# Kernel optimization log

Measured on AMD Instinct MI355X. Metric: run time of the kernel, lower is better.

The kernel has to match this reference:

```python
import jax, jax.numpy as jnp
import numpy as np

NUM_GRAPHS = 64


def gcn_conv(x, W, b, row, col, ew, n_nodes):
    # PyG GCNConv with edge weights: add self-loops (weight 1), symmetric norm.
    deg = jax.ops.segment_sum(ew, col, num_segments=n_nodes) + 1.0  # self-loop weight
    dis = jnp.where(deg > 0, jax.lax.rsqrt(deg), 0.0)
    norm = dis[row] * ew * dis[col]  # [E]
    xw = x @ W  # [N, H]
    # edge messages aggregated at target (col) + self-loop contribution dis_i^2 * xw_i
    agg = jnp.zeros_like(xw).at[col].add(norm[:, None] * xw[row])
    agg = agg + (dis * dis)[:, None] * xw
    return agg + b


def reference(x, edge_index, edge_attr, batch, W1, b1, W2, b2, actor_w, actor_b, critic_w, critic_b):
    n_nodes = x.shape[0]
    row, col = edge_index[0], edge_index[1]
    ew = jnp.abs(edge_attr)
    h = jax.nn.relu(gcn_conv(x, W1, b1, row, col, ew, n_nodes))
    # dropout p=0.1 is identity in eval mode
    h = jax.nn.relu(gcn_conv(h, W2, b2, row, col, ew, n_nodes))
    action_logits = (h @ actor_w + actor_b)[:, 0]  # [N]
    # global mean pool over graphs
    sums = jax.ops.segment_sum(h, batch, num_segments=NUM_GRAPHS)  # [G, H]
    counts = jax.ops.segment_sum(jnp.ones((n_nodes,), h.dtype), batch, num_segments=NUM_GRAPHS)
    graph_embed = sums / jnp.maximum(counts, 1.0)[:, None]
    value = graph_embed @ critic_w + critic_b  # [G, 1]
    return (action_logits, value)


def setup_inputs() -> dict:
    key = jax.random.key(0)
    ks = jax.random.split(key, 10)
    N, F, H, E = 100000, 128, 64, 1600000
    s = lambda fan: 1.0 / np.sqrt(fan)
    return {
        "x": jax.random.normal(ks[0], (N, F), jnp.float32),
        "edge_index": jax.random.randint(ks[1], (2, E), 0, N, jnp.int32),
        "edge_attr": jax.random.normal(ks[2], (E,), jnp.float32),
        "batch": jnp.sort(jax.random.randint(ks[3], (N,), 0, 64, jnp.int32)),
        "W1": jax.random.normal(ks[4], (F, H), jnp.float32) * s(F),
        "b1": jnp.zeros((H,), jnp.float32),
        "W2": jax.random.normal(ks[5], (H, H), jnp.float32) * s(H),
        "b2": jnp.zeros((H,), jnp.float32),
        "actor_w": jax.random.normal(ks[6], (H, 1), jnp.float32) * s(H),
        "actor_b": jnp.zeros((1,), jnp.float32),
        "critic_w": jax.random.normal(ks[7], (H, 1), jnp.float32) * s(H),
        "critic_b": jnp.zeros((1,), jnp.float32),
    }
```

## Files before the change

kernel.cpp:

```cpp
#include <hip/hip_runtime.h>
#include <hip/hip_fp16.h>


#define TB 256
#define BSH2 9
#define BW2 512
#define CHUNK 4096
#define NB1MAX 256
#define PAD 8

__global__ __launch_bounds__(256) void passA_k(const int* __restrict__ col,
                                               const int* __restrict__ row,
                                               const float* __restrict__ ea,
                                               int* __restrict__ gCur,
                                               uint2* __restrict__ recA,
                                               int E, int CAPB, int NB1) {
    __shared__ int hist[NB1MAX], base[NB1MAX], cur[NB1MAX];
    int t = threadIdx.x;
    int e0 = blockIdx.x * CHUNK;
    if (t < NB1MAX) { hist[t] = 0; cur[t] = 0; }
    __syncthreads();
    for (int i = t; i < CHUNK; i += 256) {
        int e = e0 + i;
        if (e < E) atomicAdd(&hist[col[e] >> BSH2], 1);
    }
    __syncthreads();
    if (t < NB1) base[t] = atomicAdd(&gCur[t], hist[t]);
    __syncthreads();
    for (int i = t; i < CHUNK; i += 256) {
        int e = e0 + i;
        if (e >= E) continue;
        int c = col[e];
        int b = c >> BSH2;
        int pos = base[b] + atomicAdd(&cur[b], 1);
        if (pos < CAPB)
            recA[(size_t)b * CAPB + pos] =
                make_uint2(((unsigned)(c & (BW2 - 1)) << 17) | (unsigned)row[e],
                           __float_as_uint(fabsf(ea[e])));
    }
}

__global__ __launch_bounds__(256) void passB_k(const int* __restrict__ gCur,
                                               const uint2* __restrict__ recA,
                                               uint2* __restrict__ rec,
                                               int* __restrict__ ptr,
                                               int* __restrict__ cnt,
                                               float* __restrict__ dis,
                                               int N, int CAPB) {
    __shared__ int hist[BW2], excl[BW2], cur[BW2];
    __shared__ float sumL[BW2];
    __shared__ int part[256];
    int b = blockIdx.x, t = threadIdx.x;
    int nrec = min(gCur[b], CAPB);
    for (int i = t; i < BW2; i += 256) { hist[i] = 0; cur[i] = 0; sumL[i] = 0.f; }
    __syncthreads();
    const uint2* ra = recA + (size_t)b * CAPB;
    for (int i = t; i < nrec; i += 256) {
        uint2 r = ra[i];
        int lc = r.x >> 17;
        atomicAdd(&hist[lc], 1);
        atomicAdd(&sumL[lc], __uint_as_float(r.y));
    }
    __syncthreads();
    int p0 = (hist[t * 2] + PAD - 1) & ~(PAD - 1);
    int p1 = (hist[t * 2 + 1] + PAD - 1) & ~(PAD - 1);
    int s = p0 + p1;
    part[t] = s;
    __syncthreads();
    for (int d = 1; d < 256; d <<= 1) {
        int v = (t >= d) ? part[t - d] : 0;
        __syncthreads();
        part[t] += v;
        __syncthreads();
    }
    int poff = t ? part[t - 1] : 0;
    excl[t * 2] = poff;
    excl[t * 2 + 1] = poff + p0;
    __syncthreads();
    for (int i = t; i < nrec; i += 256) {
        uint2 r = ra[i];
        int lc = r.x >> 17;
        int pos = atomicAdd(&cur[lc], 1);
        rec[(size_t)b * CAPB + excl[lc] + pos] = make_uint2(r.x & 0x1FFFFu, r.y);
    }
    __syncthreads();
    int c0 = b << BSH2;
    for (int i = t; i < BW2; i += 256) {
        int node = c0 + i;
        int hv = hist[i];
        int pc = (hv + PAD - 1) & ~(PAD - 1);
        for (int j = hv; j < pc; ++j)
            rec[(size_t)b * CAPB + excl[i] + j] = make_uint2(0u, 0u);
        if (node < N) {
            ptr[node] = b * CAPB + excl[i];
            cnt[node] = pc;
            dis[node] = rsqrtf(sumL[i] + 1.0f);
        }
    }
}

#define FMA_ROW(ar, xv)                                                        \
    ar.x = fmaf(xv.x, w0.x, ar.x); ar.y = fmaf(xv.x, w0.y, ar.y);              \
    ar.z = fmaf(xv.x, w0.z, ar.z); ar.w = fmaf(xv.x, w0.w, ar.w);              \
    ar.x = fmaf(xv.y, w1.x, ar.x); ar.y = fmaf(xv.y, w1.y, ar.y);              \
    ar.z = fmaf(xv.y, w1.z, ar.z); ar.w = fmaf(xv.y, w1.w, ar.w);              \
    ar.x = fmaf(xv.z, w2.x, ar.x); ar.y = fmaf(xv.z, w2.y, ar.y);              \
    ar.z = fmaf(xv.z, w2.z, ar.z); ar.w = fmaf(xv.z, w2.w, ar.w);              \
    ar.x = fmaf(xv.w, w3.x, ar.x); ar.y = fmaf(xv.w, w3.y, ar.y);              \
    ar.z = fmaf(xv.w, w3.z, ar.z); ar.w = fmaf(xv.w, w3.w, ar.w);

template <int K, typename T>
__global__ __launch_bounds__(256) void gemm_k(const T* __restrict__ X,
                                              const float* __restrict__ W,
                                              __half* __restrict__ Y, int N) {
    __shared__ float xs[64 * K];
    const int tid = threadIdx.x;
    const int row0 = blockIdx.x * 64;
    float4* xs4 = reinterpret_cast<float4*>(xs);
    if constexpr (sizeof(T) == 4) {
        const float4* X4 = reinterpret_cast<const float4*>((const float*)X + (size_t)row0 * K);
        for (int idx = tid; idx < 64 * K / 4; idx += 256) {
            int r = row0 + (idx * 4) / K;
            xs4[idx] = (r < N) ? X4[idx] : float4{0.f, 0.f, 0.f, 0.f};
        }
    } else {
        const __half2* X2 = reinterpret_cast<const __half2*>((const __half*)X + (size_t)row0 * K);
        for (int idx = tid; idx < 64 * K / 4; idx += 256) {
            int r = row0 + (idx * 4) / K;
            if (r < N) {
                float2 fa = __half22float2(X2[2 * idx]);
                float2 fb = __half22float2(X2[2 * idx + 1]);
                xs4[idx] = float4{fa.x, fa.y, fb.x, fb.y};
            } else xs4[idx] = float4{0.f, 0.f, 0.f, 0.f};
        }
    }
    __syncthreads();
    const int cg = tid & 15;
    const int rg = tid >> 4;
    const float4* W4 = reinterpret_cast<const float4*>(W);
    const float4* xr0 = reinterpret_cast<const float4*>(xs + (rg * 4 + 0) * K);
    const float4* xr1 = reinterpret_cast<const float4*>(xs + (rg * 4 + 1) * K);
    const float4* xr2 = reinterpret_cast<const float4*>(xs + (rg * 4 + 2) * K);
    const float4* xr3 = reinterpret_cast<const float4*>(xs + (rg * 4 + 3) * K);
    float4 a0 = {0.f, 0.f, 0.f, 0.f}, a1 = a0, a2 = a0, a3 = a0;
#pragma unroll 2
    for (int k4 = 0; k4 < K / 4; ++k4) {
        float4 x0 = xr0[k4], x1 = xr1[k4], x2 = xr2[k4], x3 = xr3[k4];
        float4 w0 = W4[(k4 * 4 + 0) * 16 + cg];
        float4 w1 = W4[(k4 * 4 + 1) * 16 + cg];
        float4 w2 = W4[(k4 * 4 + 2) * 16 + cg];
        float4 w3 = W4[(k4 * 4 + 3) * 16 + cg];
        FMA_ROW(a0, x0)
        FMA_ROW(a1, x1)
        FMA_ROW(a2, x2)
        FMA_ROW(a3, x3)
    }
    int r = row0 + rg * 4;
    __half2* yp0 = reinterpret_cast<__half2*>(Y + (size_t)r * 64 + cg * 4);
    if (r < N) {
        yp0[0] = __float22half2_rn(make_float2(a0.x, a0.y));
        yp0[1] = __float22half2_rn(make_float2(a0.z, a0.w));
    }
    if (r + 1 < N) {
        __half2* yp = yp0 + 32;
        yp[0] = __float22half2_rn(make_float2(a1.x, a1.y));
        yp[1] = __float22half2_rn(make_float2(a1.z, a1.w));
    }
    if (r + 2 < N) {
        __half2* yp = yp0 + 64;
        yp[0] = __float22half2_rn(make_float2(a2.x, a2.y));
        yp[1] = __float22half2_rn(make_float2(a2.z, a2.w));
    }
    if (r + 3 < N) {
        __half2* yp = yp0 + 96;
        yp[0] = __float22half2_rn(make_float2(a3.x, a3.y));
        yp[1] = __float22half2_rn(make_float2(a3.z, a3.w));
    }
}

template <bool WITH_LOGITS>
__global__ __launch_bounds__(256) void agg_fin_k(const int* __restrict__ ptr,
                                                 const int* __restrict__ cnt,
                                                 const uint2* __restrict__ rec,
                                                 const float* __restrict__ dis,
                                                 const __half2* __restrict__ xw2,
                                                 const float* __restrict__ bias,
                                                 __half2* __restrict__ hout,
                                                 const float* __restrict__ aw,
                                                 const float* __restrict__ ab,
                                                 float* __restrict__ logits, int N) {
    int n = blockIdx.x * 4 + (threadIdx.x >> 6);
    if (n >= N) return;
    int lane = threadIdx.x & 63;
    int half_id = lane >> 5;
    int fl = lane & 31;
    int base = ptr[n], num = cnt[n];
    float ax = 0.f, ay = 0.f;
    for (int k0 = 0; k0 < num; k0 += 64) {
        int rem = min(num - k0, 64);
        int r = 0; float w = 0.f;
        if (lane < rem) {
            uint2 rv = rec[(size_t)base + k0 + lane];
            r = (int)rv.x;
            w = __uint_as_float(rv.y) * dis[r];
        }
        for (int k = 0; k < rem; k += 8) {
            int i0 = k + half_id;
            int   ra0 = __shfl(r, i0),     ra1 = __shfl(r, i0 + 2);
            int   ra2 = __shfl(r, i0 + 4), ra3 = __shfl(r, i0 + 6);
            float wa0 = __shfl(w, i0),     wa1 = __shfl(w, i0 + 2);
            float wa2 = __shfl(w, i0 + 4), wa3 = __shfl(w, i0 + 6);
            __half2 v0 = xw2[(size_t)ra0 * 32 + fl];
            __half2 v1 = xw2[(size_t)ra1 * 32 + fl];
            __half2 v2 = xw2[(size_t)ra2 * 32 + fl];
            __half2 v3 = xw2[(size_t)ra3 * 32 + fl];
            float2 f;
            f = __half22float2(v0); ax = fmaf(wa0, f.x, ax); ay = fmaf(wa0, f.y, ay);
            f = __half22float2(v1); ax = fmaf(wa1, f.x, ax); ay = fmaf(wa1, f.y, ay);
            f = __half22float2(v2); ax = fmaf(wa2, f.x, ax); ay = fmaf(wa2, f.y, ay);
            f = __half22float2(v3); ax = fmaf(wa3, f.x, ax); ay = fmaf(wa3, f.y, ay);
        }
    }
    ax += __shfl(ax, lane ^ 32);
    ay += __shfl(ay, lane ^ 32);
    if (half_id == 0) {
        float d = dis[n];
        float2 xs = __half22float2(xw2[(size_t)n * 32 + fl]);
        float2 bb = reinterpret_cast<const float2*>(bias)[fl];
        float2 out;
        out.x = fmaxf(fmaf(d, fmaf(d, xs.x, ax), bb.x), 0.0f);
        out.y = fmaxf(fmaf(d, fmaf(d, xs.y, ay), bb.y), 0.0f);
        hout[(size_t)n * 32 + fl] = __float22half2_rn(out);
        if constexpr (WITH_LOGITS) {
            float2 awv = reinterpret_cast<const float2*>(aw)[fl];
            float lg = out.x * awv.x + out.y * awv.y;
            lg += __shfl(lg, lane ^ 1);
            lg += __shfl(lg, lane ^ 2);
            lg += __shfl(lg, lane ^ 4);
            lg += __shfl(lg, lane ^ 8);
            lg += __shfl(lg, lane ^ 16);
            if (lane == 0) logits[n] = lg + ab[0];
        }
    }
}

__global__ __launch_bounds__(256) void pool_k(const __half2* __restrict__ h2,
                                              const int* __restrict__ batch,
                                              float* __restrict__ sums,
                                              float* __restrict__ counts,
                                              int N, int C) {
    int wave = blockIdx.x * 4 + (threadIdx.x >> 6);
    int lane = threadIdx.x & 63;
    int start = wave * C;
    if (start >= N) return;
    if (lane >= 32) return;
    int end = min(start + C, N);
    int fl = lane;
    int cur = batch[start];
    float accx = 0.f, accy = 0.f;
    int cntv = 0;
    for (int i = start; i < end; ++i) {
        float2 v = __half22float2(h2[(size_t)i * 32 + fl]);
        int g = batch[i];
        if (g != cur) {
            atomicAdd(&sums[cur * 64 + 2 * fl], accx);
            atomicAdd(&sums[cur * 64 + 2 * fl + 1], accy);
            if (fl == 0) atomicAdd(&counts[cur], (float)cntv);
            accx = 0.f; accy = 0.f; cntv = 0; cur = g;
        }
        accx += v.x; accy += v.y; ++cntv;
    }
    atomicAdd(&sums[cur * 64 + 2 * fl], accx);
    atomicAdd(&sums[cur * 64 + 2 * fl + 1], accy);
    if (fl == 0) atomicAdd(&counts[cur], (float)cntv);
}

__global__ void value_k(const float* __restrict__ sums, const float* __restrict__ counts,
                        const float* __restrict__ cw, const float* __restrict__ cb,
                        float* __restrict__ val) {
    int g = blockIdx.x;
    int lane = threadIdx.x;
    float cntv = fmaxf(counts[g], 1.0f);
    float p = (sums[g * 64 + lane] / cntv) * cw[lane];
    for (int off = 32; off; off >>= 1) p += __shfl_down(p, off);
    if (lane == 0) val[g] = p + cb[0];
}

extern "C" void kernel_launch(void* const* d_in, const int* in_sizes, int n_in,
                              void* d_out, int out_size, void* d_ws, size_t ws_size,
                              hipStream_t stream) {
    const float* x     = (const float*)d_in[0];
    const int*   ei    = (const int*)d_in[1];
    const float* ea    = (const float*)d_in[2];
    const int*   batch = (const int*)d_in[3];
    const float* W1    = (const float*)d_in[4];
    const float* b1    = (const float*)d_in[5];
    const float* W2    = (const float*)d_in[6];
    const float* b2    = (const float*)d_in[7];
    const float* aw    = (const float*)d_in[8];
    const float* ab    = (const float*)d_in[9];
    const float* cw    = (const float*)d_in[10];
    const float* cb    = (const float*)d_in[11];

    const int N = in_sizes[3];
    const int E = in_sizes[2];
    const int H = 64, G = 64;
    const int* row = ei;
    const int* col = ei + E;

    const int NB1  = (N + BW2 - 1) >> BSH2;
    const int CAPB = (((E / NB1) * 3 / 2 + 512) + 1) & ~1;

    float*  sums   = (float*)d_ws;
    float*  counts = sums + G * H;
    int*    gCur   = (int*)(counts + G);
    float*  dis    = (float*)(gCur + NB1MAX);
    uint2*  recA   = (uint2*)(dis + N);
    uint2*  rec    = recA + (size_t)NB1 * CAPB;
    int*    ptr    = (int*)(rec + (size_t)NB1 * CAPB);
    int*    cnt    = ptr + N;
    __half* xwh    = (__half*)(cnt + N);
    __half* hbuf   = xwh + (size_t)N * H;

    float* logits = (float*)d_out;
    float* value  = logits + N;

    hipMemsetAsync(sums, 0, (size_t)(G * H + G + NB1MAX) * 4, stream);

    passA_k<<<(E + CHUNK - 1) / CHUNK, 256, 0, stream>>>(col, row, ea, gCur, recA, E, CAPB, NB1);
    passB_k<<<NB1, 256, 0, stream>>>(gCur, recA, rec, ptr, cnt, dis, N, CAPB);

    gemm_k<128, float><<<(N + 63) / 64, 256, 0, stream>>>(x, W1, xwh, N);
    agg_fin_k<false><<<(N + 3) / 4, 256, 0, stream>>>(ptr, cnt, rec, dis,
        (const __half2*)xwh, b1, (__half2*)hbuf, nullptr, nullptr, nullptr, N);

    gemm_k<64, __half><<<(N + 63) / 64, 256, 0, stream>>>(hbuf, W2, xwh, N);
    agg_fin_k<true><<<(N + 3) / 4, 256, 0, stream>>>(ptr, cnt, rec, dis,
        (const __half2*)xwh, b2, (__half2*)hbuf, aw, ab, logits, N);

    const int WAVES = 4096;
    const int C = (N + WAVES - 1) / WAVES;
    pool_k<<<WAVES / 4, 256, 0, stream>>>((const __half2*)hbuf, batch, sums, counts, N, C);
    value_k<<<G, 64, 0, stream>>>(sums, counts, cw, cb, value);
}
```

Measured before the change: 251.4 us.

## Fuse edge bucketing with first GEMM and pooling with value head

Merges the passA edge-bucketing kernel and the first dense GEMM into one launch, with block ranges split by role, so the independent stages can run side by side and one launch is removed. It also fuses the mean-pool and value kernels: the last block to finish, found through an atomic counter, computes the critic values. The agg loop gets an unroll pragma. The cost is 32KB of shared memory for the bucketing blocks too, which may limit occupancy, plus a serial 64-graph tail on a single block.

```diff
diff --git a/kernel.cpp b/kernel.cpp
--- a/kernel.cpp
+++ b/kernel.cpp
@@ -9,34 +9,101 @@
 #define NB1MAX 256
 #define PAD 8
 
-__global__ __launch_bounds__(256) void passA_k(const int* __restrict__ col,
-                                               const int* __restrict__ row,
-                                               const float* __restrict__ ea,
-                                               int* __restrict__ gCur,
-                                               uint2* __restrict__ recA,
-                                               int E, int CAPB, int NB1) {
-    __shared__ int hist[NB1MAX], base[NB1MAX], cur[NB1MAX];
-    int t = threadIdx.x;
-    int e0 = blockIdx.x * CHUNK;
-    if (t < NB1MAX) { hist[t] = 0; cur[t] = 0; }
-    __syncthreads();
-    for (int i = t; i < CHUNK; i += 256) {
-        int e = e0 + i;
-        if (e < E) atomicAdd(&hist[col[e] >> BSH2], 1);
-    }
-    __syncthreads();
-    if (t < NB1) base[t] = atomicAdd(&gCur[t], hist[t]);
-    __syncthreads();
-    for (int i = t; i < CHUNK; i += 256) {
-        int e = e0 + i;
-        if (e >= E) continue;
-        int c = col[e];
-        int b = c >> BSH2;
-        int pos = base[b] + atomicAdd(&cur[b], 1);
-        if (pos < CAPB)
-            recA[(size_t)b * CAPB + pos] =
-                make_uint2(((unsigned)(c & (BW2 - 1)) << 17) | (unsigned)row[e],
-                           __float_as_uint(fabsf(ea[e])));
+#define FMA_ROW(ar, xv)                                                        \
+    ar.x = fmaf(xv.x, w0.x, ar.x); ar.y = fmaf(xv.x, w0.y, ar.y);              \
+    ar.z = fmaf(xv.x, w0.z, ar.z); ar.w = fmaf(xv.x, w0.w, ar.w);              \
+    ar.x = fmaf(xv.y, w1.x, ar.x); ar.y = fmaf(xv.y, w1.y, ar.y);              \
+    ar.z = fmaf(xv.y, w1.z, ar.z); ar.w = fmaf(xv.y, w1.w, ar.w);              \
+    ar.x = fmaf(xv.z, w2.x, ar.x); ar.y = fmaf(xv.z, w2.y, ar.y);              \
+    ar.z = fmaf(xv.z, w2.z, ar.z); ar.w = fmaf(xv.z, w2.w, ar.w);              \
+    ar.x = fmaf(xv.w, w3.x, ar.x); ar.y = fmaf(xv.w, w3.y, ar.y);              \
+    ar.z = fmaf(xv.w, w3.z, ar.z); ar.w = fmaf(xv.w, w3.w, ar.w);
+
+__global__ __launch_bounds__(256) void buildA_gemm1_k(
+        const int* __restrict__ col, const int* __restrict__ row,
+        const float* __restrict__ ea, int* __restrict__ gCur,
+        uint2* __restrict__ recA, int E, int CAPB, int NB1, int NBA,
+        const float* __restrict__ X, const float* __restrict__ W,
+        __half* __restrict__ Y, int N) {
+    __shared__ __align__(16) char smem[64 * 128 * 4];
+    const int t = threadIdx.x;
+    if (blockIdx.x < NBA) {
+        int* hist = (int*)smem;
+        int* base = hist + NB1MAX;
+        int* cur  = base + NB1MAX;
+        int e0 = blockIdx.x * CHUNK;
+        if (t < NB1MAX) { hist[t] = 0; cur[t] = 0; }
+        __syncthreads();
+        for (int i = t; i < CHUNK; i += 256) {
+            int e = e0 + i;
+            if (e < E) atomicAdd(&hist[col[e] >> BSH2], 1);
+        }
+        __syncthreads();
+        if (t < NB1) base[t] = atomicAdd(&gCur[t], hist[t]);
+        __syncthreads();
+        for (int i = t; i < CHUNK; i += 256) {
+            int e = e0 + i;
+            if (e >= E) continue;
+            int c = col[e];
+            int b = c >> BSH2;
+            int pos = base[b] + atomicAdd(&cur[b], 1);
+            if (pos < CAPB)
+                recA[(size_t)b * CAPB + pos] =
+                    make_uint2(((unsigned)(c & (BW2 - 1)) << 17) | (unsigned)row[e],
+                               __float_as_uint(fabsf(ea[e])));
+        }
+    } else {
+        const int K = 128;
+        float* xs = (float*)smem;
+        const int row0 = (blockIdx.x - NBA) * 64;
+        float4* xs4 = reinterpret_cast<float4*>(xs);
+        const float4* X4 = reinterpret_cast<const float4*>(X + (size_t)row0 * K);
+        for (int idx = t; idx < 64 * K / 4; idx += 256) {
+            int r = row0 + (idx * 4) / K;
+            xs4[idx] = (r < N) ? X4[idx] : float4{0.f, 0.f, 0.f, 0.f};
+        }
+        __syncthreads();
+        const int cg = t & 15;
+        const int rg = t >> 4;
+        const float4* W4 = reinterpret_cast<const float4*>(W);
+        const float4* xr0 = reinterpret_cast<const float4*>(xs + (rg * 4 + 0) * K);
+        const float4* xr1 = reinterpret_cast<const float4*>(xs + (rg * 4 + 1) * K);
+        const float4* xr2 = reinterpret_cast<const float4*>(xs + (rg * 4 + 2) * K);
+        const float4* xr3 = reinterpret_cast<const float4*>(xs + (rg * 4 + 3) * K);
+        float4 a0 = {0.f, 0.f, 0.f, 0.f}, a1 = a0, a2 = a0, a3 = a0;
+#pragma unroll 2
+        for (int k4 = 0; k4 < K / 4; ++k4) {
+            float4 x0 = xr0[k4], x1 = xr1[k4], x2 = xr2[k4], x3 = xr3[k4];
+            float4 w0 = W4[(k4 * 4 + 0) * 16 + cg];
+            float4 w1 = W4[(k4 * 4 + 1) * 16 + cg];
+            float4 w2 = W4[(k4 * 4 + 2) * 16 + cg];
+            float4 w3 = W4[(k4 * 4 + 3) * 16 + cg];
+            FMA_ROW(a0, x0)
+            FMA_ROW(a1, x1)
+            FMA_ROW(a2, x2)
+            FMA_ROW(a3, x3)
+        }
+        int r = row0 + rg * 4;
+        __half2* yp0 = reinterpret_cast<__half2*>(Y + (size_t)r * 64 + cg * 4);
+        if (r < N) {
+            yp0[0] = __float22half2_rn(make_float2(a0.x, a0.y));
+            yp0[1] = __float22half2_rn(make_float2(a0.z, a0.w));
+        }
+        if (r + 1 < N) {
+            __half2* yp = yp0 + 32;
+            yp[0] = __float22half2_rn(make_float2(a1.x, a1.y));
+            yp[1] = __float22half2_rn(make_float2(a1.z, a1.w));
+        }
+        if (r + 2 < N) {
+            __half2* yp = yp0 + 64;
+            yp[0] = __float22half2_rn(make_float2(a2.x, a2.y));
+            yp[1] = __float22half2_rn(make_float2(a2.z, a2.w));
+        }
+        if (r + 3 < N) {
+            __half2* yp = yp0 + 96;
+            yp[0] = __float22half2_rn(make_float2(a3.x, a3.y));
+            yp[1] = __float22half2_rn(make_float2(a3.z, a3.w));
+        }
     }
 }
 
@@ -99,40 +166,22 @@
     }
 }
 
-#define FMA_ROW(ar, xv)                                                        \
-    ar.x = fmaf(xv.x, w0.x, ar.x); ar.y = fmaf(xv.x, w0.y, ar.y);              \
-    ar.z = fmaf(xv.x, w0.z, ar.z); ar.w = fmaf(xv.x, w0.w, ar.w);              \
-    ar.x = fmaf(xv.y, w1.x, ar.x); ar.y = fmaf(xv.y, w1.y, ar.y);              \
-    ar.z = fmaf(xv.y, w1.z, ar.z); ar.w = fmaf(xv.y, w1.w, ar.w);              \
-    ar.x = fmaf(xv.z, w2.x, ar.x); ar.y = fmaf(xv.z, w2.y, ar.y);              \
-    ar.z = fmaf(xv.z, w2.z, ar.z); ar.w = fmaf(xv.z, w2.w, ar.w);              \
-    ar.x = fmaf(xv.w, w3.x, ar.x); ar.y = fmaf(xv.w, w3.y, ar.y);              \
-    ar.z = fmaf(xv.w, w3.z, ar.z); ar.w = fmaf(xv.w, w3.w, ar.w);
-
-template <int K, typename T>
-__global__ __launch_bounds__(256) void gemm_k(const T* __restrict__ X,
-                                              const float* __restrict__ W,
-                                              __half* __restrict__ Y, int N) {
+__global__ __launch_bounds__(256) void gemm2_k(const __half* __restrict__ X,
+                                               const float* __restrict__ W,
+                                               __half* __restrict__ Y, int N) {
+    const int K = 64;
     __shared__ float xs[64 * K];
     const int tid = threadIdx.x;
     const int row0 = blockIdx.x * 64;
     float4* xs4 = reinterpret_cast<float4*>(xs);
-    if constexpr (sizeof(T) == 4) {
-        const float4* X4 = reinterpret_cast<const float4*>((const float*)X + (size_t)row0 * K);
-        for (int idx = tid; idx < 64 * K / 4; idx += 256) {
-            int r = row0 + (idx * 4) / K;
-            xs4[idx] = (r < N) ? X4[idx] : float4{0.f, 0.f, 0.f, 0.f};
-        }
-    } else {
-        const __half2* X2 = reinterpret_cast<const __half2*>((const __half*)X + (size_t)row0 * K);
-        for (int idx = tid; idx < 64 * K / 4; idx += 256) {
-            int r = row0 + (idx * 4) / K;
-            if (r < N) {
-                float2 fa = __half22float2(X2[2 * idx]);
-                float2 fb = __half22float2(X2[2 * idx + 1]);
-                xs4[idx] = float4{fa.x, fa.y, fb.x, fb.y};
-            } else xs4[idx] = float4{0.f, 0.f, 0.f, 0.f};
-        }
+    const __half2* X2 = reinterpret_cast<const __half2*>(X + (size_t)row0 * K);
+    for (int idx = tid; idx < 64 * K / 4; idx += 256) {
+        int r = row0 + (idx * 4) / K;
+        if (r < N) {
+            float2 fa = __half22float2(X2[2 * idx]);
+            float2 fb = __half22float2(X2[2 * idx + 1]);
+            xs4[idx] = float4{fa.x, fa.y, fb.x, fb.y};
+        } else xs4[idx] = float4{0.f, 0.f, 0.f, 0.f};
     }
     __syncthreads();
     const int cg = tid & 15;
@@ -204,6 +253,7 @@
             r = (int)rv.x;
             w = __uint_as_float(rv.y) * dis[r];
         }
+#pragma unroll 2
         for (int k = 0; k < rem; k += 8) {
             int i0 = k + half_id;
             int   ra0 = __shfl(r, i0),     ra1 = __shfl(r, i0 + 2);
@@ -244,46 +294,54 @@
     }
 }
 
-__global__ __launch_bounds__(256) void pool_k(const __half2* __restrict__ h2,
-                                              const int* __restrict__ batch,
-                                              float* __restrict__ sums,
-                                              float* __restrict__ counts,
-                                              int N, int C) {
+__global__ __launch_bounds__(256) void pool_value_k(const __half2* __restrict__ h2,
+                                                    const int* __restrict__ batch,
+                                                    float* __restrict__ sums,
+                                                    float* __restrict__ counts,
+                                                    int* __restrict__ done,
+                                                    const float* __restrict__ cw,
+                                                    const float* __restrict__ cb,
+                                                    float* __restrict__ val,
+                                                    int N, int C, int NBLK) {
     int wave = blockIdx.x * 4 + (threadIdx.x >> 6);
     int lane = threadIdx.x & 63;
     int start = wave * C;
-    if (start >= N) return;
-    if (lane >= 32) return;
-    int end = min(start + C, N);
-    int fl = lane;
-    int cur = batch[start];
-    float accx = 0.f, accy = 0.f;
-    int cntv = 0;
-    for (int i = start; i < end; ++i) {
-        float2 v = __half22float2(h2[(size_t)i * 32 + fl]);
-        int g = batch[i];
-        if (g != cur) {
-            atomicAdd(&sums[cur * 64 + 2 * fl], accx);
-            atomicAdd(&sums[cur * 64 + 2 * fl + 1], accy);
-            if (fl == 0) atomicAdd(&counts[cur], (float)cntv);
-            accx = 0.f; accy = 0.f; cntv = 0; cur = g;
-        }
-        accx += v.x; accy += v.y; ++cntv;
-    }
-    atomicAdd(&sums[cur * 64 + 2 * fl], accx);
-    atomicAdd(&sums[cur * 64 + 2 * fl + 1], accy);
-    if (fl == 0) atomicAdd(&counts[cur], (float)cntv);
-}
-
-__global__ void value_k(const float* __restrict__ sums, const float* __restrict__ counts,
-                        const float* __restrict__ cw, const float* __restrict__ cb,
-                        float* __restrict__ val) {
-    int g = blockIdx.x;
-    int lane = threadIdx.x;
-    float cntv = fmaxf(counts[g], 1.0f);
-    float p = (sums[g * 64 + lane] / cntv) * cw[lane];
-    for (int off = 32; off; off >>= 1) p += __shfl_down(p, off);
-    if (lane == 0) val[g] = p + cb[0];
+    if (start < N && lane < 32) {
+        int end = min(start + C, N);
+        int fl = lane;
+        int cur = batch[start];
+        float accx = 0.f, accy = 0.f;
+        int cntv = 0;
+        for (int i = start; i < end; ++i) {
+            float2 v = __half22float2(h2[(size_t)i * 32 + fl]);
+            int g = batch[i];
+            if (g != cur) {
+                atomicAdd(&sums[cur * 64 + 2 * fl], accx);
+                atomicAdd(&sums[cur * 64 + 2 * fl + 1], accy);
+                if (fl == 0) atomicAdd(&counts[cur], (float)cntv);
+                accx = 0.f; accy = 0.f; cntv = 0; cur = g;
+            }
+            accx += v.x; accy += v.y; ++cntv;
+        }
+        atomicAdd(&sums[cur * 64 + 2 * fl], accx);
+        atomicAdd(&sums[cur * 64 + 2 * fl + 1], accy);
+        if (fl == 0) atomicAdd(&counts[cur], (float)cntv);
+    }
+    __threadfence();
+    __syncthreads();
+    __shared__ int lastB;
+    if (threadIdx.x == 0) lastB = (atomicAdd(done, 1) == NBLK - 1) ? 1 : 0;
+    __syncthreads();
+    if (lastB && threadIdx.x < 64) {
+        __threadfence();
+        int l = threadIdx.x;
+        for (int g = 0; g < 64; ++g) {
+            float cv = fmaxf(atomicAdd(&counts[g], 0.0f), 1.0f);
+            float p = (atomicAdd(&sums[g * 64 + l], 0.0f) / cv) * cw[l];
+            for (int off = 32; off; off >>= 1) p += __shfl_down(p, off);
+            if (l == 0) val[g] = p + cb[0];
+        }
+    }
 }
 
 extern "C" void kernel_launch(void* const* d_in, const int* in_sizes, int n_in,
@@ -310,11 +368,14 @@
 
     const int NB1  = (N + BW2 - 1) >> BSH2;
     const int CAPB = (((E / NB1) * 3 / 2 + 512) + 1) & ~1;
+    const int NBA  = (E + CHUNK - 1) / CHUNK;
+    const int NG1  = (N + 63) / 64;
 
     float*  sums   = (float*)d_ws;
     float*  counts = sums + G * H;
     int*    gCur   = (int*)(counts + G);
-    float*  dis    = (float*)(gCur + NB1MAX);
+    int*    done   = gCur + NB1MAX;
+    float*  dis    = (float*)(done + 2);
     uint2*  recA   = (uint2*)(dis + N);
     uint2*  rec    = recA + (size_t)NB1 * CAPB;
     int*    ptr    = (int*)(rec + (size_t)NB1 * CAPB);
@@ -325,21 +386,23 @@
     float* logits = (float*)d_out;
     float* value  = logits + N;
 
-    hipMemsetAsync(sums, 0, (size_t)(G * H + G + NB1MAX) * 4, stream);
-
-    passA_k<<<(E + CHUNK - 1) / CHUNK, 256, 0, stream>>>(col, row, ea, gCur, recA, E, CAPB, NB1);
+    hipMemsetAsync(sums, 0, (size_t)(G * H + G + NB1MAX + 2) * 4, stream);
+
+    buildA_gemm1_k<<<NBA + NG1, 256, 0, stream>>>(col, row, ea, gCur, recA,
+                                                  E, CAPB, NB1, NBA,
+                                                  x, W1, xwh, N);
     passB_k<<<NB1, 256, 0, stream>>>(gCur, recA, rec, ptr, cnt, dis, N, CAPB);
 
-    gemm_k<128, float><<<(N + 63) / 64, 256, 0, stream>>>(x, W1, xwh, N);
     agg_fin_k<false><<<(N + 3) / 4, 256, 0, stream>>>(ptr, cnt, rec, dis,
         (const __half2*)xwh, b1, (__half2*)hbuf, nullptr, nullptr, nullptr, N);
 
-    gemm_k<64, __half><<<(N + 63) / 64, 256, 0, stream>>>(hbuf, W2, xwh, N);
+    gemm2_k<<<(N + 63) / 64, 256, 0, stream>>>(hbuf, W2, xwh, N);
     agg_fin_k<true><<<(N + 3) / 4, 256, 0, stream>>>(ptr, cnt, rec, dis,
         (const __half2*)xwh, b2, (__half2*)hbuf, aw, ab, logits, N);
 
     const int WAVES = 4096;
     const int C = (N + WAVES - 1) / WAVES;
-    pool_k<<<WAVES / 4, 256, 0, stream>>>((const __half2*)hbuf, batch, sums, counts, N, C);
-    value_k<<<G, 64, 0, stream>>>(sums, counts, cw, cb, value);
-}
+    const int NBLK = WAVES / 4;
+    pool_value_k<<<NBLK, 256, 0, stream>>>((const __half2*)hbuf, batch, sums,
+                                           counts, done, cw, cb, value, N, C, NBLK);
+}
```

After: 330.2 us. 1.31x slower.
